# Kernel optimization log

Measured on AMD Instinct MI355X. Metric: run time of the kernel, lower is better.

Reference implementation:

```python
import jax, jax.numpy as jnp
import numpy as np

B, N, CQ, CH, H = 2, 2048, 256, 256, 8
D = CH // H  # head_dim = 32


def setup_inputs() -> dict:
    key = jax.random.key(0)
    ks = jax.random.split(key, 10)
    s = 0.02
    return {
        "q_x": jax.random.normal(ks[0], (B, N, CQ), dtype=jnp.float32),
        "attn_bias": jax.random.normal(ks[1], (B, H, N, N), dtype=jnp.float32),
        "Wq": jax.random.normal(ks[2], (CQ, CH), dtype=jnp.float32) * s,
        "bq": jnp.zeros((CH,), dtype=jnp.float32),
        "Wk": jax.random.normal(ks[3], (CQ, CH), dtype=jnp.float32) * s,
        "Wv": jax.random.normal(ks[4], (CQ, CH), dtype=jnp.float32) * s,
        "Wout": jax.random.normal(ks[5], (CH, CQ), dtype=jnp.float32) * s,
        "bout": jnp.zeros((CQ,), dtype=jnp.float32),
        "Wg": jax.random.normal(ks[6], (CQ, CQ), dtype=jnp.float32) * s,
        "bg": jnp.zeros((CQ,), dtype=jnp.float32),
        "gbias": jnp.ones((CQ,), dtype=jnp.float32),
    }


def reference(q_x, attn_bias, Wq, bq, Wk, Wv, Wout, bout, Wg, bg, gbias):
    # prep_qkv: project, split heads; scale q by 1/sqrt(head_dim) (apply_scale path)
    scale = 1.0 / jnp.sqrt(jnp.asarray(D, q_x.dtype))
    q = ((q_x @ Wq + bq).reshape(B, N, H, D)) * scale  # [B,N,H,D]
    k = (q_x @ Wk).reshape(B, N, H, D)
    v = (q_x @ Wv).reshape(B, N, H, D)
    # attention with additive pair bias
    scores = jnp.einsum("bqhd,bkhd->bhqk", q, k) + attn_bias  # [B,H,N,N]
    attn = jax.nn.softmax(scores, axis=-1)
    o = jnp.einsum("bhqk,bkhd->bqhd", attn, v).reshape(B, N, CH)  # merge heads
    # wrap_up: output projection + sigmoid gate (gating_bias init ones)
    out = o @ Wout + bout  # [B,N,CQ]
    gate = jax.nn.sigmoid(q_x @ Wg + bg + gbias)
    return gate * out
```

## Files before the change

kernel.cpp:

```cpp
#include <hip/hip_runtime.h>

typedef __bf16 bf16_t;
typedef bf16_t bf16x8 __attribute__((ext_vector_type(8)));
typedef float f32x4 __attribute__((ext_vector_type(4)));
typedef unsigned short ushort8 __attribute__((ext_vector_type(8)));

#define LOG2E 1.4426950408889634f

static __device__ __forceinline__ unsigned short f2bf(float f) {
  union { float f; unsigned u; } a; a.f = f;
  unsigned r = a.u + 0x7FFFu + ((a.u >> 16) & 1u);
  return (unsigned short)(r >> 16);
}

static __device__ __forceinline__ bf16x8 ldb8(const unsigned short* p) {
  return *reinterpret_cast<const bf16x8*>(p);
}

__global__ __launch_bounds__(256) void proj_k(
    const float* __restrict__ X, const float* __restrict__ bq,
    const float* __restrict__ Wq, const float* __restrict__ Wk,
    const float* __restrict__ Wv,
    unsigned short* __restrict__ q_ws, unsigned short* __restrict__ k_ws,
    unsigned short* __restrict__ vt_ws) {
  __shared__ unsigned short wl[64][264];
  __shared__ unsigned short vtile[64][72];
  const int tid = threadIdx.x;
  const int wave = tid >> 6, l = tid & 63, g = l >> 4, l15 = l & 15;
  const int mrow = blockIdx.x * 64 + wave * 16 + l15;
  const int widx = blockIdx.y >> 2;
  const int nin0 = (blockIdx.y & 3) * 64;
  const float* W = (widx == 0) ? Wq : (widx == 1) ? Wk : Wv;

  {
    const int c = tid & 63;
#pragma unroll
    for (int kk = tid >> 6; kk < 256; kk += 4)
      wl[c][kk] = f2bf(W[kk * 256 + nin0 + c]);
  }
  __syncthreads();

  f32x4 acc[4];
#pragma unroll
  for (int st = 0; st < 4; ++st) acc[st] = f32x4{0.f, 0.f, 0.f, 0.f};

#pragma unroll
  for (int kk0 = 0; kk0 < 256; kk0 += 32) {
    const float* xp = X + mrow * 256 + kk0 + 8 * g;
    f32x4 x0 = *reinterpret_cast<const f32x4*>(xp);
    f32x4 x1 = *reinterpret_cast<const f32x4*>(xp + 4);
    union { unsigned short u[8]; bf16x8 v; } av;
#pragma unroll
    for (int e = 0; e < 4; ++e) { av.u[e] = f2bf(x0[e]); av.u[4 + e] = f2bf(x1[e]); }
#pragma unroll
    for (int st = 0; st < 4; ++st) {
      bf16x8 bv = ldb8(&wl[st * 16 + l15][kk0 + 8 * g]);
      acc[st] = __builtin_amdgcn_mfma_f32_16x16x32_bf16(av.v, bv, acc[st], 0, 0, 0);
    }
  }

  const int mb = blockIdx.x * 64 + wave * 16 + 4 * g;
  if (widx == 2) {
#pragma unroll
    for (int st = 0; st < 4; ++st)
#pragma unroll
      for (int j = 0; j < 4; ++j)
        vtile[st * 16 + l15][wave * 16 + 4 * g + j] = f2bf(acc[st][j]);
    __syncthreads();
    const int b = (blockIdx.x * 64) >> 11;
    const int t0 = (blockIdx.x * 64) & 2047;
#pragma unroll
    for (int it = tid; it < 512; it += 256) {
      const int r = it >> 3, cseg = (it & 7) * 8;
      const int n = nin0 + r;
      *reinterpret_cast<ushort8*>(vt_ws + (size_t)((b * 8 + (n >> 5)) * 32 + (n & 31)) * 2048 +
                                  t0 + cseg) = *reinterpret_cast<const ushort8*>(&vtile[r][cseg]);
    }
  } else {
#pragma unroll
    for (int st = 0; st < 4; ++st) {
      const int n = nin0 + st * 16 + l15;
      const int h = n >> 5, d = n & 31;
#pragma unroll
      for (int j = 0; j < 4; ++j) {
        const int m = mb + j;
        const int b = m >> 11, t = m & 2047;
        if (widx == 0) {
          q_ws[((b * 8 + h) * 2048 + t) * 32 + d] =
              f2bf((acc[st][j] + bq[n]) * (0.17677669529663687f * LOG2E));
        } else {
          k_ws[((b * 8 + h) * 2048 + t) * 32 + d] = f2bf(acc[st][j]);
        }
      }
    }
  }
}

__global__ __launch_bounds__(256, 3) void attn_k(
    const unsigned short* __restrict__ q_ws, const unsigned short* __restrict__ k_ws,
    const unsigned short* __restrict__ vt_ws, const float* __restrict__ bias,
    unsigned short* __restrict__ o_ws) {
  __shared__ float sbias[4][2][1024];
  __shared__ unsigned short plds[4][16 * 72];
  const int tid = threadIdx.x;
  const int wave = tid >> 6, l = tid & 63, g = l >> 4, l15 = l & 15;
  const int bh = blockIdx.x >> 5, qt = blockIdx.x & 31;
  const int qr0 = qt * 64 + wave * 16;
  const int kvbase = bh * 2048;
  unsigned short* pw = plds[wave];

  const bf16x8 qa = ldb8(q_ws + (size_t)(kvbase + qr0 + l15) * 32 + 8 * g);
  const unsigned short* kbase = k_ws + (size_t)kvbase * 32 + 8 * g + l15 * 32;
  const unsigned short* vbase = vt_ws + (size_t)(bh * 32 + l15) * 2048 + 8 * g;
  const float* bsrc = bias + ((size_t)bh << 22) + (size_t)(qr0 + (l >> 4)) * 2048 + (l & 15) * 4;

  auto stage = [&](int buf, int k0) {
    float* dst = &sbias[wave][buf][0];
#pragma unroll
    for (int qq = 0; qq < 4; ++qq)
      __builtin_amdgcn_global_load_lds(
          (const __attribute__((address_space(1))) void*)(bsrc + (size_t)qq * 8192 + k0),
          (__attribute__((address_space(3))) void*)(dst + qq * 256), 16, 0, 0);
  };

  float mr[4], lr[4];
  f32x4 oacc[2];
#pragma unroll
  for (int j = 0; j < 4; ++j) { mr[j] = -1e30f; lr[j] = 0.0f; }
  oacc[0] = f32x4{0.f, 0.f, 0.f, 0.f};
  oacc[1] = f32x4{0.f, 0.f, 0.f, 0.f};

  stage(0, 0);
#pragma unroll 1
  for (int kt = 0; kt < 32; ++kt) {
    const int buf = kt & 1;
    const int k0 = kt * 64;
    asm volatile("s_waitcnt vmcnt(0)" ::: "memory");
    __builtin_amdgcn_sched_barrier(0);
    f32x4 cfr[4];
    const float* sbc = &sbias[wave][buf][0] + l15;
#pragma unroll
    for (int st = 0; st < 4; ++st)
#pragma unroll
      for (int j = 0; j < 4; ++j)
        cfr[st][j] = sbc[(4 * g + j) * 64 + st * 16] * LOG2E;

    bf16x8 kb[4];
#pragma unroll
    for (int st = 0; st < 4; ++st) kb[st] = ldb8(kbase + (size_t)(k0 + st * 16) * 32);
    bf16x8 vb[2][2];
#pragma unroll
    for (int dst = 0; dst < 2; ++dst)
#pragma unroll
      for (int kc = 0; kc < 2; ++kc)
        vb[dst][kc] = ldb8(vbase + (size_t)dst * 16 * 2048 + k0 + kc * 32);

    if (kt < 31) stage(buf ^ 1, k0 + 64);

    f32x4 s[4];
#pragma unroll
    for (int st = 0; st < 4; ++st)
      s[st] = __builtin_amdgcn_mfma_f32_16x16x32_bf16(qa, kb[st], cfr[st], 0, 0, 0);

#pragma unroll
    for (int j = 0; j < 4; ++j) {
      float mx = fmaxf(fmaxf(s[0][j], s[1][j]), fmaxf(s[2][j], s[3][j]));
      mx = fmaxf(mx, __shfl_xor(mx, 1));
      mx = fmaxf(mx, __shfl_xor(mx, 2));
      mx = fmaxf(mx, __shfl_xor(mx, 4));
      mx = fmaxf(mx, __shfl_xor(mx, 8));
      const float mn = fmaxf(mr[j], mx);
      const float sc = __builtin_amdgcn_exp2f(mr[j] - mn);
      mr[j] = mn;
      float rs = 0.f;
#pragma unroll
      for (int st = 0; st < 4; ++st) {
        float e = __builtin_amdgcn_exp2f(s[st][j] - mn);
        s[st][j] = e;
        rs += e;
      }
      rs += __shfl_xor(rs, 1);
      rs += __shfl_xor(rs, 2);
      rs += __shfl_xor(rs, 4);
      rs += __shfl_xor(rs, 8);
      lr[j] = lr[j] * sc + rs;
      oacc[0][j] *= sc;
      oacc[1][j] *= sc;
    }
#pragma unroll
    for (int st = 0; st < 4; ++st)
#pragma unroll
      for (int j = 0; j < 4; ++j)
        pw[(4 * g + j) * 72 + st * 16 + l15] = f2bf(s[st][j]);
#pragma unroll
    for (int kc = 0; kc < 2; ++kc) {
      bf16x8 pa = ldb8(pw + l15 * 72 + kc * 32 + 8 * g);
      oacc[0] = __builtin_amdgcn_mfma_f32_16x16x32_bf16(pa, vb[0][kc], oacc[0], 0, 0, 0);
      oacc[1] = __builtin_amdgcn_mfma_f32_16x16x32_bf16(pa, vb[1][kc], oacc[1], 0, 0, 0);
    }
  }

  const int b = bh >> 3, h = bh & 7;
#pragma unroll
  for (int dst = 0; dst < 2; ++dst)
#pragma unroll
    for (int j = 0; j < 4; ++j) {
      const int q = qr0 + 4 * g + j;
      const float val = oacc[dst][j] / lr[j];
      o_ws[((size_t)(b * 2048 + q)) * 256 + h * 32 + dst * 16 + l15] = f2bf(val);
    }
}

__global__ __launch_bounds__(256) void outp_k(
    const unsigned short* __restrict__ o_ws, const float* __restrict__ X,
    const float* __restrict__ Wg, const float* __restrict__ Wo,
    const float* __restrict__ bout, const float* __restrict__ bg,
    const float* __restrict__ gbias, float* __restrict__ out) {
  __shared__ unsigned short wgl[64][264];
  __shared__ unsigned short wol[64][264];
  const int tid = threadIdx.x;
  const int wave = tid >> 6, l = tid & 63, g = l >> 4, l15 = l & 15;
  const int m0 = blockIdx.x * 64 + wave * 16;
  const int c0 = blockIdx.y * 64;

  {
    const int c = tid & 63;
#pragma unroll
    for (int kk = tid >> 6; kk < 256; kk += 4) {
      wgl[c][kk] = f2bf(Wg[kk * 256 + c0 + c]);
      wol[c][kk] = f2bf(Wo[kk * 256 + c0 + c]);
    }
  }
  __syncthreads();

  f32x4 acco[4], accg[4];
#pragma unroll
  for (int st = 0; st < 4; ++st) {
    acco[st] = f32x4{0.f, 0.f, 0.f, 0.f};
    accg[st] = f32x4{0.f, 0.f, 0.f, 0.f};
  }
#pragma unroll
  for (int kk0 = 0; kk0 < 256; kk0 += 32) {
    const bf16x8 a_o = ldb8(o_ws + (m0 + l15) * 256 + kk0 + 8 * g);
    const float* xp = X + (m0 + l15) * 256 + kk0 + 8 * g;
    f32x4 x0 = *reinterpret_cast<const f32x4*>(xp);
    f32x4 x1 = *reinterpret_cast<const f32x4*>(xp + 4);
    union { unsigned short u[8]; bf16x8 v; } av;
#pragma unroll
    for (int e = 0; e < 4; ++e) { av.u[e] = f2bf(x0[e]); av.u[4 + e] = f2bf(x1[e]); }
#pragma unroll
    for (int st = 0; st < 4; ++st) {
      bf16x8 bo = ldb8(&wol[st * 16 + l15][kk0 + 8 * g]);
      acco[st] = __builtin_amdgcn_mfma_f32_16x16x32_bf16(a_o, bo, acco[st], 0, 0, 0);
      bf16x8 bgf = ldb8(&wgl[st * 16 + l15][kk0 + 8 * g]);
      accg[st] = __builtin_amdgcn_mfma_f32_16x16x32_bf16(av.v, bgf, accg[st], 0, 0, 0);
    }
  }
  const int mb = m0 + 4 * g;
#pragma unroll
  for (int st = 0; st < 4; ++st) {
    const int n = c0 + st * 16 + l15;
#pragma unroll
    for (int j = 0; j < 4; ++j) {
      const int m = mb + j;
      const float z = accg[st][j] + bg[n] + gbias[n];
      const float gate = 1.0f / (1.0f + __expf(-z));
      out[m * 256 + n] = gate * (acco[st][j] + bout[n]);
    }
  }
}

extern "C" void kernel_launch(void* const* d_in, const int* in_sizes, int n_in,
                              void* d_out, int out_size, void* d_ws, size_t ws_size,
                              hipStream_t stream) {
  const float* q_x   = (const float*)d_in[0];
  const float* bias  = (const float*)d_in[1];
  const float* Wq    = (const float*)d_in[2];
  const float* bq    = (const float*)d_in[3];
  const float* Wk    = (const float*)d_in[4];
  const float* Wv    = (const float*)d_in[5];
  const float* Wout  = (const float*)d_in[6];
  const float* bout  = (const float*)d_in[7];
  const float* Wg    = (const float*)d_in[8];
  const float* bg    = (const float*)d_in[9];
  const float* gbias = (const float*)d_in[10];
  float* out = (float*)d_out;

  char* ws = (char*)d_ws;
  unsigned short* q_ws  = (unsigned short*)(ws);
  unsigned short* k_ws  = (unsigned short*)(ws + 2097152);
  unsigned short* vt_ws = (unsigned short*)(ws + 2 * 2097152);
  unsigned short* o_ws  = (unsigned short*)(ws + 3 * 2097152);

  proj_k<<<dim3(64, 12), 256, 0, stream>>>(q_x, bq, Wq, Wk, Wv, q_ws, k_ws, vt_ws);
  attn_k<<<512, 256, 0, stream>>>(q_ws, k_ws, vt_ws, bias, o_ws);
  outp_k<<<dim3(64, 4), 256, 0, stream>>>(o_ws, q_x, Wg, Wout, bout, bg, gbias, out);
}
```

Measured before the change: 95.33 us.

## Split attention over the key dimension and merge partials in a combine kernel

```diff
diff --git a/kernel.cpp b/kernel.cpp
--- a/kernel.cpp
+++ b/kernel.cpp
@@ -96,18 +96,21 @@
   }
 }
 
-__global__ __launch_bounds__(256, 3) void attn_k(
+__global__ __launch_bounds__(256, 4) void attn_k(
     const unsigned short* __restrict__ q_ws, const unsigned short* __restrict__ k_ws,
     const unsigned short* __restrict__ vt_ws, const float* __restrict__ bias,
-    unsigned short* __restrict__ o_ws) {
+    float* __restrict__ p_o, float* __restrict__ p_ml) {
   __shared__ float sbias[4][2][1024];
-  __shared__ unsigned short plds[4][16 * 72];
   const int tid = threadIdx.x;
   const int wave = tid >> 6, l = tid & 63, g = l >> 4, l15 = l & 15;
-  const int bh = blockIdx.x >> 5, qt = blockIdx.x & 31;
+  const int bid = blockIdx.x;
+  const int nb = (bid & 7) * 128 + (bid >> 3);
+  const int bh = nb >> 6;
+  const int qt = (nb & 63) >> 1;
+  const int split = nb & 1;
+  const int koff = split << 10;
   const int qr0 = qt * 64 + wave * 16;
   const int kvbase = bh * 2048;
-  unsigned short* pw = plds[wave];
 
   const bf16x8 qa = ldb8(q_ws + (size_t)(kvbase + qr0 + l15) * 32 + 8 * g);
   const unsigned short* kbase = k_ws + (size_t)kvbase * 32 + 8 * g + l15 * 32;
@@ -130,11 +133,11 @@
   oacc[0] = f32x4{0.f, 0.f, 0.f, 0.f};
   oacc[1] = f32x4{0.f, 0.f, 0.f, 0.f};
 
-  stage(0, 0);
+  stage(0, koff);
 #pragma unroll 1
-  for (int kt = 0; kt < 32; ++kt) {
+  for (int kt = 0; kt < 16; ++kt) {
     const int buf = kt & 1;
-    const int k0 = kt * 64;
+    const int k0 = koff + kt * 64;
     asm volatile("s_waitcnt vmcnt(0)" ::: "memory");
     __builtin_amdgcn_sched_barrier(0);
     f32x4 cfr[4];
@@ -155,7 +158,7 @@
       for (int kc = 0; kc < 2; ++kc)
         vb[dst][kc] = ldb8(vbase + (size_t)dst * 16 * 2048 + k0 + kc * 32);
 
-    if (kt < 31) stage(buf ^ 1, k0 + 64);
+    if (kt < 15) stage(buf ^ 1, k0 + 64);
 
     f32x4 s[4];
 #pragma unroll
@@ -187,6 +190,7 @@
       oacc[0][j] *= sc;
       oacc[1][j] *= sc;
     }
+    unsigned short* pw = (unsigned short*)&sbias[wave][buf][0];
 #pragma unroll
     for (int st = 0; st < 4; ++st)
 #pragma unroll
@@ -200,15 +204,38 @@
     }
   }
 
+  const int rowbase = kvbase + qr0;
+  float* po = p_o + ((size_t)split * 32768 + rowbase) * 32;
+#pragma unroll
+  for (int dst = 0; dst < 2; ++dst)
+#pragma unroll
+    for (int j = 0; j < 4; ++j)
+      po[(4 * g + j) * 32 + dst * 16 + l15] = oacc[dst][j];
+  if (l15 == 0) {
+#pragma unroll
+    for (int j = 0; j < 4; ++j) {
+      const size_t r = (size_t)split * 32768 + rowbase + 4 * g + j;
+      p_ml[r * 2] = mr[j];
+      p_ml[r * 2 + 1] = lr[j];
+    }
+  }
+}
+
+__global__ __launch_bounds__(256) void combine_k(
+    const float* __restrict__ p_o, const float* __restrict__ p_ml,
+    unsigned short* __restrict__ o_ws) {
+  const int gid = blockIdx.x * 256 + threadIdx.x;
+  const int row = gid >> 5, d = gid & 31;
+  const float m0 = p_ml[row * 2], l0 = p_ml[row * 2 + 1];
+  const float m1 = p_ml[(32768 + row) * 2], l1 = p_ml[(32768 + row) * 2 + 1];
+  const float m = fmaxf(m0, m1);
+  const float w0 = __builtin_amdgcn_exp2f(m0 - m), w1 = __builtin_amdgcn_exp2f(m1 - m);
+  const float o0 = p_o[(size_t)row * 32 + d];
+  const float o1 = p_o[(size_t)(32768 + row) * 32 + d];
+  const float val = (o0 * w0 + o1 * w1) / (l0 * w0 + l1 * w1);
+  const int bh = row >> 11, q = row & 2047;
   const int b = bh >> 3, h = bh & 7;
-#pragma unroll
-  for (int dst = 0; dst < 2; ++dst)
-#pragma unroll
-    for (int j = 0; j < 4; ++j) {
-      const int q = qr0 + 4 * g + j;
-      const float val = oacc[dst][j] / lr[j];
-      o_ws[((size_t)(b * 2048 + q)) * 256 + h * 32 + dst * 16 + l15] = f2bf(val);
-    }
+  o_ws[((size_t)(b * 2048 + q)) * 256 + h * 32 + d] = f2bf(val);
 }
 
 __global__ __launch_bounds__(256) void outp_k(
@@ -291,8 +318,11 @@
   unsigned short* k_ws  = (unsigned short*)(ws + 2097152);
   unsigned short* vt_ws = (unsigned short*)(ws + 2 * 2097152);
   unsigned short* o_ws  = (unsigned short*)(ws + 3 * 2097152);
+  float* p_o            = (float*)(ws + 4 * 2097152);
+  float* p_ml           = (float*)(ws + 8 * 2097152);
 
   proj_k<<<dim3(64, 12), 256, 0, stream>>>(q_x, bq, Wq, Wk, Wv, q_ws, k_ws, vt_ws);
-  attn_k<<<512, 256, 0, stream>>>(q_ws, k_ws, vt_ws, bias, o_ws);
+  attn_k<<<1024, 256, 0, stream>>>(q_ws, k_ws, vt_ws, bias, p_o, p_ml);
+  combine_k<<<4096, 256, 0, stream>>>(p_o, p_ml, o_ws);
   outp_k<<<dim3(64, 4), 256, 0, stream>>>(o_ws, q_x, Wg, Wout, bout, bg, gbias, out);
 }
```

Measured after the change: 106.8 us. 12.0% more time.
